# Performance work log

Hardware: AMD Instinct MI355X
Metric: run time of the kernel (lower is better)

## Reference

```python
import jax, jax.numpy as jnp
import numpy as np

IN_FEATURES = 4096
OUT_FEATURES = 4096
NNZ = 1677722
TOKENS = 8192


def setup_inputs() -> dict:
    key = jax.random.key(0)
    k_x, k_val, k_row, k_col, k_b = jax.random.split(key, 5)
    x = jax.random.normal(k_x, (TOKENS, IN_FEATURES), dtype=jnp.float32)
    values = jax.random.normal(k_val, (NNZ,), dtype=jnp.float32)
    row_ids = jax.random.randint(k_row, (NNZ,), 0, OUT_FEATURES, dtype=jnp.int32)
    col_ids = jax.random.randint(k_col, (NNZ,), 0, IN_FEATURES, dtype=jnp.int32)
    bias = jax.random.normal(k_b, (OUT_FEATURES,), dtype=jnp.float32)
    return {"x": x, "values": values, "row_ids": row_ids, "col_ids": col_ids, "bias": bias}


def reference(x, values, row_ids, col_ids, bias):
    # F.linear(input, W_sparse, bias) == x @ W^T + bias where W is the
    # (out_features, in_features) sparse weight. Materialize W from its
    # nonzeros with a scatter-add (duplicate coords sum, matching sparse semantics),
    # then use a single dense matmul.
    out_f = bias.shape[0]
    in_f = x.shape[-1]
    W = jnp.zeros((out_f, in_f), dtype=x.dtype).at[row_ids, col_ids].add(values)
    return x @ W.T + bias
```

## Files before the change

kernel.cpp:

```cpp
#include <hip/hip_runtime.h>
#include <hip/hip_bf16.h>
#include <stdint.h>

#define IN_F 4096
#define OUT_F 4096
#define NTOK 8192

typedef __attribute__((ext_vector_type(8))) __bf16 bf16x8;
typedef __attribute__((ext_vector_type(4))) float f32x4;

__device__ __forceinline__ unsigned short f2bf(float f) {
    unsigned u = __float_as_uint(f);
    u += 0x7fffu + ((u >> 16) & 1u);
    return (unsigned short)(u >> 16);
}

__global__ void scatter_kernel(const float* __restrict__ vals,
                               const int* __restrict__ rows,
                               const int* __restrict__ cols,
                               float* __restrict__ W, int nnz) {
    int i = blockIdx.x * blockDim.x + threadIdx.x;
    if (i < nnz) atomicAdd(&W[(size_t)rows[i] * IN_F + cols[i]], vals[i]);
}

__global__ void cvt2_kernel(const float4* __restrict__ a, ushort4* __restrict__ oa, int na4,
                            const float4* __restrict__ b, ushort4* __restrict__ ob, int nb4) {
    int stride = gridDim.x * blockDim.x;
    int tot = na4 + nb4;
    for (int i = blockIdx.x * blockDim.x + threadIdx.x; i < tot; i += stride) {
        const float4* src; ushort4* dst; int j;
        if (i < na4) { src = a; dst = oa; j = i; }
        else         { src = b; dst = ob; j = i - na4; }
        float4 v = src[j];
        ushort4 o;
        o.x = f2bf(v.x); o.y = f2bf(v.y); o.z = f2bf(v.z); o.w = f2bf(v.w);
        dst[j] = o;
    }
}

#define GLD_LDS16(gp, lp)                                              \
    __builtin_amdgcn_global_load_lds(                                  \
        (__attribute__((address_space(1))) void*)(void*)(gp),          \
        (__attribute__((address_space(3))) void*)(lp), 16, 0, 0)

#define STAGE(tt) do {                                                 \
    const int _b = ((tt) & 3) * 16384;                                 \
    const size_t _k = (size_t)(tt) * 32;                               \
    GLD_LDS16(A0 + _k, &lds[_b + ldst0]);                              \
    GLD_LDS16(A1 + _k, &lds[_b + ldst1]);                              \
    GLD_LDS16(B0 + _k, &lds[_b + 8192 + ldst0]);                       \
    GLD_LDS16(B1 + _k, &lds[_b + 8192 + ldst1]);                       \
} while (0)

template<int VM>
__device__ __forceinline__ void kiter(int t,
        const ushort* __restrict__ A0, const ushort* __restrict__ A1,
        const ushort* __restrict__ B0, const ushort* __restrict__ B1,
        ushort* lds, int ldst0, int ldst1,
        const int (&aoff)[8], const int (&boff)[4], f32x4 (&acc)[8][4]) {
    if constexpr (VM == 8)      asm volatile("s_waitcnt vmcnt(8)" ::: "memory");
    else if constexpr (VM == 4) asm volatile("s_waitcnt vmcnt(4)" ::: "memory");
    else                        asm volatile("s_waitcnt vmcnt(0)" ::: "memory");
    __builtin_amdgcn_s_barrier();
    if (t + 3 < IN_F / 32) STAGE(t + 3);
    const int bb = (t & 3) * 16384;
    bf16x8 af[8], bg[4];
#pragma unroll
    for (int m = 0; m < 8; ++m) af[m] = *(const bf16x8*)&lds[bb + aoff[m]];
#pragma unroll
    for (int n = 0; n < 4; ++n) bg[n] = *(const bf16x8*)&lds[bb + 8192 + boff[n]];
    __builtin_amdgcn_s_setprio(1);
#pragma unroll
    for (int m = 0; m < 8; ++m)
#pragma unroll
        for (int n = 0; n < 4; ++n)
            acc[m][n] = __builtin_amdgcn_mfma_f32_16x16x32_bf16(af[m], bg[n], acc[m][n], 0, 0, 0);
    __builtin_amdgcn_s_setprio(0);
}

__global__ __launch_bounds__(512, 2)
void gemm_bt_bias(const ushort* __restrict__ A,
                  const ushort* __restrict__ B,
                  const float* __restrict__ bias,
                  float* __restrict__ C) {
    constexpr int N = OUT_F, K = IN_F;
    constexpr int NT = K / 32;

    extern __shared__ ushort lds[];

    const int tid  = threadIdx.x;
    const int lane = tid & 63;
    const int wid  = tid >> 6;

    const int bid = blockIdx.x;
    const int nb  = (bid & 7) * 64 + (bid >> 3);
    const int by = nb >> 4, bx = nb & 15;
    const int brow = by * 256, bcol = bx * 256;

    const int wr = wid >> 2, wc = wid & 3;

    const int d0 = tid * 8, d1 = (512 + tid) * 8;
    const int s0 = d0 ^ (((d0 >> 6) & 7) << 3);
    const int s1 = d1 ^ (((d1 >> 6) & 7) << 3);
    const ushort* A0 = A + (size_t)(brow + (s0 >> 5)) * K + (s0 & 31);
    const ushort* A1 = A + (size_t)(brow + (s1 >> 5)) * K + (s1 & 31);
    const ushort* B0 = B + (size_t)(bcol + (s0 >> 5)) * K + (s0 & 31);
    const ushort* B1 = B + (size_t)(bcol + (s1 >> 5)) * K + (s1 & 31);
    const int ldst0 = (wid * 64) * 8;
    const int ldst1 = (512 + wid * 64) * 8;

    const int fr = lane & 15, kq = (lane >> 4) * 8;
    int aoff[8], boff[4];
#pragma unroll
    for (int m = 0; m < 8; ++m) {
        int lin = (wr * 128 + m * 16 + fr) * 32 + kq;
        aoff[m] = lin ^ (((lin >> 6) & 7) << 3);
    }
#pragma unroll
    for (int n = 0; n < 4; ++n) {
        int lin = (wc * 64 + n * 16 + fr) * 32 + kq;
        boff[n] = lin ^ (((lin >> 6) & 7) << 3);
    }

    f32x4 acc[8][4] = {};

    STAGE(0); STAGE(1); STAGE(2);

    for (int t = 0; t < NT - 2; ++t)
        kiter<8>(t, A0, A1, B0, B1, lds, ldst0, ldst1, aoff, boff, acc);
    kiter<4>(NT - 2, A0, A1, B0, B1, lds, ldst0, ldst1, aoff, boff, acc);
    kiter<0>(NT - 1, A0, A1, B0, B1, lds, ldst0, ldst1, aoff, boff, acc);

    const int crow0 = brow + wr * 128;
    const int ccol0 = bcol + wc * 64;
#pragma unroll
    for (int n = 0; n < 4; ++n) {
        const int col = ccol0 + n * 16 + fr;
        const float bv = bias[col];
#pragma unroll
        for (int m = 0; m < 8; ++m) {
            const int r0 = crow0 + m * 16 + (lane >> 4) * 4;
#pragma unroll
            for (int j = 0; j < 4; ++j)
                C[(size_t)(r0 + j) * N + col] = acc[m][n][j] + bv;
        }
    }
}

extern "C" void kernel_launch(void* const* d_in, const int* in_sizes, int n_in,
                              void* d_out, int out_size, void* d_ws, size_t ws_size,
                              hipStream_t stream) {
    const float* x    = (const float*)d_in[0];
    const float* vals = (const float*)d_in[1];
    const int*   rows = (const int*)d_in[2];
    const int*   cols = (const int*)d_in[3];
    const float* bias = (const float*)d_in[4];
    float* out = (float*)d_out;
    const int nnz = in_sizes[1];

    char* ws = (char*)d_ws;
    float*  Wf = (float*)ws;
    ushort* Wb = (ushort*)(ws + (size_t)64 * 1024 * 1024);
    ushort* Xb = (ushort*)(ws + (size_t)96 * 1024 * 1024);

    hipMemsetAsync(Wf, 0, (size_t)OUT_F * IN_F * sizeof(float), stream);
    scatter_kernel<<<(nnz + 255) / 256, 256, 0, stream>>>(vals, rows, cols, Wf, nnz);
    cvt2_kernel<<<4096, 256, 0, stream>>>((const float4*)Wf, (ushort4*)Wb, OUT_F * IN_F / 4,
                                          (const float4*)x,  (ushort4*)Xb, NTOK * IN_F / 4);
    gemm_bt_bias<<<dim3((NTOK / 256) * (OUT_F / 256)), 512, 131072, stream>>>(Xb, Wb, bias, out);
}
```

Measured before the change: 551.5 us.

## Interleave GEMM prefetch with MFMA groups and overlap scatter with x conversion

The GEMM k-iteration now splits its MFMA work into four pairs of m-rows. LDS fragment reads and one global-to-LDS prefetch are placed before each pair, with extra barriers between them so memory issue interleaves with matrix math instead of being front-loaded. The preprocessing is also restructured: a custom zero kernel replaces the memset, the atomic scatter runs in the same launch as the x-to-bf16 conversion on disjoint block ranges, and W is converted in its own kernel afterwards. The extra s_barrier instructions add synchronisation overhead per k-step in exchange for better interleaving.

```diff
diff --git a/kernel.cpp b/kernel.cpp
--- a/kernel.cpp
+++ b/kernel.cpp
@@ -15,26 +15,41 @@
     return (unsigned short)(u >> 16);
 }
 
-__global__ void scatter_kernel(const float* __restrict__ vals,
-                               const int* __restrict__ rows,
-                               const int* __restrict__ cols,
-                               float* __restrict__ W, int nnz) {
-    int i = blockIdx.x * blockDim.x + threadIdx.x;
-    if (i < nnz) atomicAdd(&W[(size_t)rows[i] * IN_F + cols[i]], vals[i]);
-}
-
-__global__ void cvt2_kernel(const float4* __restrict__ a, ushort4* __restrict__ oa, int na4,
-                            const float4* __restrict__ b, ushort4* __restrict__ ob, int nb4) {
+__global__ void zero_kernel(float4* __restrict__ p, int n4) {
     int stride = gridDim.x * blockDim.x;
-    int tot = na4 + nb4;
-    for (int i = blockIdx.x * blockDim.x + threadIdx.x; i < tot; i += stride) {
-        const float4* src; ushort4* dst; int j;
-        if (i < na4) { src = a; dst = oa; j = i; }
-        else         { src = b; dst = ob; j = i - na4; }
-        float4 v = src[j];
+    float4 z = {0.f, 0.f, 0.f, 0.f};
+    for (int i = blockIdx.x * blockDim.x + threadIdx.x; i < n4; i += stride) p[i] = z;
+}
+
+#define SCAT_BLOCKS 2048
+__global__ void scatter_cvtx_kernel(const float* __restrict__ vals,
+                                    const int* __restrict__ rows,
+                                    const int* __restrict__ cols,
+                                    float* __restrict__ W, int nnz,
+                                    const float4* __restrict__ x4,
+                                    ushort4* __restrict__ xb4, int nx4) {
+    if (blockIdx.x < SCAT_BLOCKS) {
+        int stride = SCAT_BLOCKS * 256;
+        for (int i = blockIdx.x * 256 + threadIdx.x; i < nnz; i += stride)
+            atomicAdd(&W[(size_t)rows[i] * IN_F + cols[i]], vals[i]);
+    } else {
+        int stride = (gridDim.x - SCAT_BLOCKS) * 256;
+        for (int i = (blockIdx.x - SCAT_BLOCKS) * 256 + threadIdx.x; i < nx4; i += stride) {
+            float4 v = x4[i];
+            ushort4 o;
+            o.x = f2bf(v.x); o.y = f2bf(v.y); o.z = f2bf(v.z); o.w = f2bf(v.w);
+            xb4[i] = o;
+        }
+    }
+}
+
+__global__ void cvtw_kernel(const float4* __restrict__ in, ushort4* __restrict__ out, int n4) {
+    int stride = gridDim.x * blockDim.x;
+    for (int i = blockIdx.x * blockDim.x + threadIdx.x; i < n4; i += stride) {
+        float4 v = in[i];
         ushort4 o;
         o.x = f2bf(v.x); o.y = f2bf(v.y); o.z = f2bf(v.z); o.w = f2bf(v.w);
-        dst[j] = o;
+        out[i] = o;
     }
 }
 
@@ -52,30 +67,63 @@
     GLD_LDS16(B1 + _k, &lds[_b + 8192 + ldst1]);                       \
 } while (0)
 
+#define PBAR() asm volatile("s_barrier" ::: "memory")
+
+#define MFMA_PAIR(m0_)                                                         \
+    do {                                                                       \
+        __builtin_amdgcn_s_setprio(1);                                         \
+        _Pragma("unroll")                                                      \
+        for (int n = 0; n < 4; ++n)                                            \
+            acc[m0_][n] = __builtin_amdgcn_mfma_f32_16x16x32_bf16(af[m0_], bg[n], acc[m0_][n], 0, 0, 0); \
+        _Pragma("unroll")                                                      \
+        for (int n = 0; n < 4; ++n)                                            \
+            acc[m0_ + 1][n] = __builtin_amdgcn_mfma_f32_16x16x32_bf16(af[m0_ + 1], bg[n], acc[m0_ + 1][n], 0, 0, 0); \
+        __builtin_amdgcn_s_setprio(0);                                         \
+    } while (0)
+
 template<int VM>
 __device__ __forceinline__ void kiter(int t,
         const ushort* __restrict__ A0, const ushort* __restrict__ A1,
         const ushort* __restrict__ B0, const ushort* __restrict__ B1,
         ushort* lds, int ldst0, int ldst1,
         const int (&aoff)[8], const int (&boff)[4], f32x4 (&acc)[8][4]) {
-    if constexpr (VM == 8)      asm volatile("s_waitcnt vmcnt(8)" ::: "memory");
-    else if constexpr (VM == 4) asm volatile("s_waitcnt vmcnt(4)" ::: "memory");
-    else                        asm volatile("s_waitcnt vmcnt(0)" ::: "memory");
-    __builtin_amdgcn_s_barrier();
-    if (t + 3 < IN_F / 32) STAGE(t + 3);
+    if constexpr (VM == 8)      asm volatile("s_waitcnt vmcnt(8)\n\ts_barrier" ::: "memory");
+    else if constexpr (VM == 4) asm volatile("s_waitcnt vmcnt(4)\n\ts_barrier" ::: "memory");
+    else                        asm volatile("s_waitcnt vmcnt(0)\n\ts_barrier" ::: "memory");
+
     const int bb = (t & 3) * 16384;
+    const int sb = ((t + 3) & 3) * 16384;
+    const size_t sk = (size_t)(t + 3) * 32;
+    const bool pf = (t + 3) < (IN_F / 32);
     bf16x8 af[8], bg[4];
-#pragma unroll
-    for (int m = 0; m < 8; ++m) af[m] = *(const bf16x8*)&lds[bb + aoff[m]];
-#pragma unroll
-    for (int n = 0; n < 4; ++n) bg[n] = *(const bf16x8*)&lds[bb + 8192 + boff[n]];
-    __builtin_amdgcn_s_setprio(1);
-#pragma unroll
-    for (int m = 0; m < 8; ++m)
-#pragma unroll
-        for (int n = 0; n < 4; ++n)
-            acc[m][n] = __builtin_amdgcn_mfma_f32_16x16x32_bf16(af[m], bg[n], acc[m][n], 0, 0, 0);
-    __builtin_amdgcn_s_setprio(0);
+
+    bg[0] = *(const bf16x8*)&lds[bb + 8192 + boff[0]];
+    bg[1] = *(const bf16x8*)&lds[bb + 8192 + boff[1]];
+    bg[2] = *(const bf16x8*)&lds[bb + 8192 + boff[2]];
+    bg[3] = *(const bf16x8*)&lds[bb + 8192 + boff[3]];
+    af[0] = *(const bf16x8*)&lds[bb + aoff[0]];
+    af[1] = *(const bf16x8*)&lds[bb + aoff[1]];
+    if (pf) GLD_LDS16(A0 + sk, &lds[sb + ldst0]);
+    PBAR();
+    MFMA_PAIR(0);
+    PBAR();
+    af[2] = *(const bf16x8*)&lds[bb + aoff[2]];
+    af[3] = *(const bf16x8*)&lds[bb + aoff[3]];
+    if (pf) GLD_LDS16(A1 + sk, &lds[sb + ldst1]);
+    PBAR();
+    MFMA_PAIR(2);
+    PBAR();
+    af[4] = *(const bf16x8*)&lds[bb + aoff[4]];
+    af[5] = *(const bf16x8*)&lds[bb + aoff[5]];
+    if (pf) GLD_LDS16(B0 + sk, &lds[sb + 8192 + ldst0]);
+    PBAR();
+    MFMA_PAIR(4);
+    PBAR();
+    af[6] = *(const bf16x8*)&lds[bb + aoff[6]];
+    af[7] = *(const bf16x8*)&lds[bb + aoff[7]];
+    if (pf) GLD_LDS16(B1 + sk, &lds[sb + 8192 + ldst1]);
+    PBAR();
+    MFMA_PAIR(6);
 }
 
 __global__ __launch_bounds__(512, 2)
@@ -163,9 +211,10 @@
     ushort* Wb = (ushort*)(ws + (size_t)64 * 1024 * 1024);
     ushort* Xb = (ushort*)(ws + (size_t)96 * 1024 * 1024);
 
-    hipMemsetAsync(Wf, 0, (size_t)OUT_F * IN_F * sizeof(float), stream);
-    scatter_kernel<<<(nnz + 255) / 256, 256, 0, stream>>>(vals, rows, cols, Wf, nnz);
-    cvt2_kernel<<<4096, 256, 0, stream>>>((const float4*)Wf, (ushort4*)Wb, OUT_F * IN_F / 4,
-                                          (const float4*)x,  (ushort4*)Xb, NTOK * IN_F / 4);
+    zero_kernel<<<2048, 256, 0, stream>>>((float4*)Wf, OUT_F * IN_F / 4);
+    scatter_cvtx_kernel<<<4096, 256, 0, stream>>>(vals, rows, cols, Wf, nnz,
+                                                  (const float4*)x, (ushort4*)Xb,
+                                                  NTOK * IN_F / 4);
+    cvtw_kernel<<<2048, 256, 0, stream>>>((const float4*)Wf, (ushort4*)Wb, OUT_F * IN_F / 4);
     gemm_bt_bias<<<dim3((NTOK / 256) * (OUT_F / 256)), 512, 131072, stream>>>(Xb, Wb, bias, out);
 }
```

Measured after the change: 577.8 us. 4.8% more time.
